# Kernel tuning notes

Measured on AMD Instinct MI355X. Metric: run time of the kernel, lower is better.

## Reference

```python
import jax, jax.numpy as jnp
import numpy as np

NUM_HEADS = 16
NEG = -10000000.0


def setup_inputs() -> dict:
    key = jax.random.key(0)
    k1, k2, k3 = jax.random.split(key, 3)
    B, N, C = 4, 2048, 1024
    inputs = jax.random.normal(k1, (B, N, C), dtype=jnp.float32)
    # learned params (xavier-ish scale)
    W_qkv = jax.random.normal(k2, (C, 3 * C), dtype=jnp.float32) * 0.02
    W_proj = jax.random.normal(k3, (C, C), dtype=jnp.float32) * 0.02
    b_proj = jnp.zeros((C,), dtype=jnp.float32)
    attn_mask = jnp.ones((N, N), dtype=jnp.int32)      # >0 means keep
    padding_mask = jnp.zeros((B, N), dtype=jnp.int32)  # >0 means mask out
    return {"inputs": inputs, "attn_mask": attn_mask, "padding_mask": padding_mask,
            "W_qkv": W_qkv, "W_proj": W_proj, "b_proj": b_proj}


def reference(inputs, attn_mask, padding_mask, W_qkv, W_proj, b_proj):
    B, N, C = inputs.shape
    H = NUM_HEADS
    d = C // H
    scale = d ** -0.5
    qkv = inputs @ W_qkv                                   # [B,N,3C]
    qkv = qkv.reshape(B, N, 3, H, d).transpose(2, 0, 3, 1, 4)  # [3,B,H,N,d]
    q, k, v = qkv[0], qkv[1], qkv[2]
    scores = jnp.einsum('bhqd,bhkd->bhqk', q, k) * scale   # [B,H,N,N]
    scores = jnp.where(attn_mask > 0, scores, NEG)
    pm = padding_mask[:, None, None, :]                    # [B,1,1,N]
    scores = jnp.where(pm > 0, NEG, scores)
    attn = jax.nn.softmax(scores, axis=-1)
    x = jnp.einsum('bhqk,bhkd->bhqd', attn, v)             # [B,H,N,d]
    x = x.swapaxes(1, 2).reshape(B, N, C)
    return x @ W_proj + b_proj
```

## Files before the change

### kernel.cpp

```cpp
#include <hip/hip_runtime.h>

#define NEG -10000000.0f
#define QSCALE 0.18033688011112042f

typedef __attribute__((ext_vector_type(8))) short bf16x8;
typedef __attribute__((ext_vector_type(4))) float f32x4;

static __device__ __forceinline__ short f2bf(float f) {
    unsigned int u = __float_as_uint(f);
    unsigned int r = (u + 0x7fffu + ((u >> 16) & 1u)) >> 16;
    return (short)r;
}

static __device__ __forceinline__ unsigned pack_bf16_2(float a, float b) {
    unsigned ua = __float_as_uint(a) + 0x8000u;
    unsigned ub = __float_as_uint(b) + 0x8000u;
    return __builtin_amdgcn_perm(ub, ua, 0x07060302u);
}

static __device__ __forceinline__ void async_cp16(const void* g, void* l) {
    __builtin_amdgcn_global_load_lds(
        (const __attribute__((address_space(1))) unsigned int*)g,
        (__attribute__((address_space(3))) unsigned int*)l, 16, 0, 0);
}

__global__ void cvt_bf16(const float* __restrict__ src, short* __restrict__ dst, int n4) {
    int i = blockIdx.x * blockDim.x + threadIdx.x;
    if (i < n4) {
        float4 v = reinterpret_cast<const float4*>(src)[i];
        short4 o;
        o.x = f2bf(v.x); o.y = f2bf(v.y); o.z = f2bf(v.z); o.w = f2bf(v.w);
        reinterpret_cast<short4*>(dst)[i] = o;
    }
}

__global__ void transpose_cvt(const float* __restrict__ src, short* __restrict__ dst,
                              int rows, int cols) {
    __shared__ float tile[32][33];
    int bx = blockIdx.x * 32;
    int by = blockIdx.y * 32;
    int tx = threadIdx.x & 31, ty = threadIdx.x >> 5;
    for (int j = 0; j < 4; ++j)
        tile[ty + j * 8][tx] = src[(size_t)(by + ty + j * 8) * cols + bx + tx];
    __syncthreads();
    for (int j = 0; j < 4; ++j)
        dst[(size_t)(bx + ty + j * 8) * rows + by + tx] = f2bf(tile[tx][ty + j * 8]);
}

__global__ void mask_flags(const int* __restrict__ attn_mask,
                           const int* __restrict__ padding, int* __restrict__ flags) {
    int blk = blockIdx.x;
    int tid = threadIdx.x;
    if (blk == 512) {
        if (tid < 128) {
            int b = tid >> 5, kt = tid & 31;
            int any = 0;
            for (int j = 0; j < 64; ++j) any |= (padding[b * 2048 + kt * 64 + j] > 0);
            flags[512 + tid] = any;
        }
        return;
    }
    int qt = blk >> 5, kt = blk & 31;
    __shared__ int blockok;
    if (tid == 0) blockok = 1;
    __syncthreads();
    int ok = 1;
    for (int j = 0; j < 32; ++j) {
        int idx = j * 256 + tid;
        int qr = qt * 128 + (idx >> 6);
        int kc = kt * 64 + (idx & 63);
        ok &= (attn_mask[(size_t)qr * 2048 + kc] != 0);
    }
    if (!ok) blockok = 0;
    __syncthreads();
    if (tid == 0) flags[blk] = blockok;
}

__global__ __launch_bounds__(256, 2) void gemm_bf16(
    const short* __restrict__ A, const short* __restrict__ Bt, int mode,
    short* __restrict__ q_ws, short* __restrict__ k_ws, short* __restrict__ v_ws,
    float* __restrict__ out, const float* __restrict__ bias) {
    const int K = 1024;
    __shared__ __align__(16) short smem[2][128][64];
    short (*As)[64] = smem[0];
    short (*Bs)[64] = smem[1];
    int tid = threadIdx.x, lane = tid & 63, w = tid >> 6;
    int wm = w & 1, wn = w >> 1;

    int nwg = gridDim.x * gridDim.y;
    int hw = blockIdx.y * gridDim.x + blockIdx.x;
    int logical = (hw & 7) * (nwg >> 3) + (hw >> 3);
    int bx = logical % gridDim.x, by = logical / gridDim.x;
    int m0 = by * 128, n0 = bx * 128;

    int col = lane & 15, quad = lane >> 4;
    int l8 = lane >> 3, j8 = lane & 7;

    f32x4 acc[4][4] = {};

    for (int k0 = 0; k0 < K; k0 += 64) {
        for (int c = 0; c < 4; ++c) {
            int rr = w * 32 + c * 8 + l8;
            int sw = (j8 ^ (rr & 7)) << 3;
            async_cp16(&A[(size_t)(m0 + rr) * K + k0 + sw], &As[w * 32 + c * 8][0]);
            async_cp16(&Bt[(size_t)(n0 + rr) * K + k0 + sw], &Bs[w * 32 + c * 8][0]);
        }
        __syncthreads();
        for (int ks = 0; ks < 2; ++ks) {
            bf16x8 af[4], bfr[4];
            for (int mt = 0; mt < 4; ++mt)
                af[mt] = *reinterpret_cast<const bf16x8*>(
                    &As[wm * 64 + mt * 16 + col][((ks * 4 + quad) ^ (col & 7)) << 3]);
            for (int nt = 0; nt < 4; ++nt)
                bfr[nt] = *reinterpret_cast<const bf16x8*>(
                    &Bs[wn * 64 + nt * 16 + col][((ks * 4 + quad) ^ (col & 7)) << 3]);
            for (int mt = 0; mt < 4; ++mt)
                for (int nt = 0; nt < 4; ++nt)
                    acc[mt][nt] = __builtin_amdgcn_mfma_f32_16x16x32_bf16(af[mt], bfr[nt], acc[mt][nt], 0, 0, 0);
        }
        __syncthreads();
    }

    short* L = &smem[0][0][0];

    if (mode == 0) {
        int which = n0 >> 10;
        int cb = n0 & 1023;
        int b = m0 >> 11, nb = m0 & 2047, hb = cb >> 6;
        if (which == 2) {
            for (int mt = 0; mt < 4; ++mt)
                for (int nt = 0; nt < 4; ++nt) {
                    int ml = wm * 64 + mt * 16 + quad * 4;
                    int cl = wn * 64 + nt * 16 + col;
                    int mp = (ml + 8 * cl) & 127;
                    short4 pk;
                    for (int r = 0; r < 4; ++r) ((short*)&pk)[r] = f2bf(acc[mt][nt][r]);
                    *reinterpret_cast<short4*>(&L[cl * 128 + mp]) = pk;
                }
            __syncthreads();
            for (int it = 0; it < 8; ++it) {
                int chunk = it * 256 + tid;
                int c = chunk >> 4, j = chunk & 15;
                int h = hb + (c >> 6), dd = c & 63;
                int4 val = *reinterpret_cast<const int4*>(&L[c * 128 + (((j + c) & 15) << 3)]);
                *reinterpret_cast<int4*>(
                    &v_ws[((size_t)((b * 16 + h) * 64 + dd)) * 2048 + nb + j * 8]) = val;
            }
        } else {
            short* dst = (which == 0) ? q_ws : k_ws;
            float scl = (which == 0) ? QSCALE : 1.0f;
            for (int mt = 0; mt < 4; ++mt)
                for (int nt = 0; nt < 4; ++nt)
                    for (int r = 0; r < 4; ++r) {
                        int ml = wm * 64 + mt * 16 + quad * 4 + r;
                        int cl = wn * 64 + nt * 16 + col;
                        L[ml * 128 + ((cl + 8 * ml) & 127)] = f2bf(acc[mt][nt][r] * scl);
                    }
            __syncthreads();
            for (int it = 0; it < 8; ++it) {
                int chunk = it * 256 + tid;
                int row = chunk >> 4, j = chunk & 15;
                int h = hb + (j >> 3), dd = (j & 7) * 8;
                int4 val = *reinterpret_cast<const int4*>(&L[row * 128 + (((j + row) & 15) << 3)]);
                *reinterpret_cast<int4*>(
                    &dst[((size_t)(b * 16 + h) * 2048 + nb + row) * 64 + dd]) = val;
            }
        }
    } else {
        float* Lf = reinterpret_cast<float*>(L);
        for (int half = 0; half < 2; ++half) {
            if (wm == half) {
                for (int mt = 0; mt < 4; ++mt)
                    for (int nt = 0; nt < 4; ++nt)
                        for (int r = 0; r < 4; ++r) {
                            int ml = mt * 16 + quad * 4 + r;
                            int cl = wn * 64 + nt * 16 + col;
                            Lf[ml * 128 + cl] = acc[mt][nt][r];
                        }
            }
            __syncthreads();
            for (int it = 0; it < 8; ++it) {
                int chunk = it * 256 + tid;
                int row = chunk >> 5, j = chunk & 31;
                float4 val = *reinterpret_cast<const float4*>(&Lf[row * 128 + j * 4]);
                float4 bv = *reinterpret_cast<const float4*>(&bias[n0 + j * 4]);
                val.x += bv.x; val.y += bv.y; val.z += bv.z; val.w += bv.w;
                *reinterpret_cast<float4*>(
                    &out[(size_t)(m0 + half * 64 + row) * 1024 + n0 + j * 4]) = val;
            }
            __syncthreads();
        }
    }
}

__global__ __launch_bounds__(256, 4) void flash_attn(
    const short* __restrict__ q_ws, const short* __restrict__ k_ws,
    const short* __restrict__ v_ws, const int* __restrict__ aflags,
    const int* __restrict__ pflags, const int* __restrict__ padding,
    const int* __restrict__ attn_mask, short* __restrict__ xb) {
    const int Nn = 2048, D = 64;
    __shared__ __align__(16) short QP[128][64];
    __shared__ __align__(16) short Ks[2][64][64];
    __shared__ __align__(16) short Vt[64][64];

    int tid = threadIdx.x, lane = tid & 63, w = tid >> 6;
    int col = lane & 15, quad = lane >> 4;

    int hw = blockIdx.y * 16 + blockIdx.x;
    int logical = (hw & 7) * 128 + (hw >> 3);
    int bh = logical >> 4, qt = logical & 15;
    int b = bh >> 4, h = bh & 15;
    int q0 = qt * 128;

    int l8 = lane >> 3, j8 = lane & 7;

    unsigned amask = (unsigned)__ballot(aflags[qt * 32 + (lane & 31)] != 0);
    unsigned pmask = (unsigned)__ballot(pflags[b * 32 + (lane & 31)] != 0);

    for (int c = 0; c < 4; ++c) {
        int rr = w * 32 + c * 8 + l8;
        async_cp16(&q_ws[((size_t)bh * Nn + q0 + rr) * D + ((j8 ^ (rr & 7)) << 3)],
                   &QP[w * 32 + c * 8][0]);
    }
    {
        int rr0 = w * 16 + l8, rr1 = w * 16 + 8 + l8;
        int s0 = (j8 ^ (rr0 & 7)) << 3, s1 = (j8 ^ (rr1 & 7)) << 3;
        async_cp16(&k_ws[((size_t)bh * Nn + rr0) * D + s0], &Ks[0][w * 16][0]);
        async_cp16(&k_ws[((size_t)bh * Nn + rr1) * D + s1], &Ks[0][w * 16 + 8][0]);
        async_cp16(&v_ws[((size_t)bh * D + rr0) * Nn + s0], &Vt[w * 16][0]);
        async_cp16(&v_ws[((size_t)bh * D + rr1) * Nn + s1], &Vt[w * 16 + 8][0]);
    }
    __syncthreads();

    bf16x8 qf[2][2];
    for (int t = 0; t < 2; ++t)
        for (int ks = 0; ks < 2; ++ks)
            qf[t][ks] = *reinterpret_cast<const bf16x8*>(
                &QP[w * 32 + t * 16 + col][((ks * 4 + quad) ^ (col & 7)) << 3]);

    f32x4 oacc[2][4] = {};
    f32x4 lacc[2] = {};

    for (int kt = 0; kt < 32; ++kt) {
        int k0 = kt * 64;
        int ktn = (kt < 31) ? kt + 1 : 31;

        if (kt) {
            asm volatile("s_waitcnt vmcnt(2)" ::: "memory");
            __builtin_amdgcn_s_barrier();
            __builtin_amdgcn_sched_barrier(0);
        }
        const short (*Kc)[64] = Ks[kt & 1];

        f32x4 sacc[4][2] = {};
        for (int ks = 0; ks < 2; ++ks) {
            bf16x8 kf[4];
            for (int mt = 0; mt < 4; ++mt)
                kf[mt] = *reinterpret_cast<const bf16x8*>(
                    &Kc[mt * 16 + col][((ks * 4 + quad) ^ (col & 7)) << 3]);
            __builtin_amdgcn_s_setprio(1);
            for (int mt = 0; mt < 4; ++mt)
                for (int t = 0; t < 2; ++t)
                    sacc[mt][t] = __builtin_amdgcn_mfma_f32_16x16x32_bf16(kf[mt], qf[t][ks], sacc[mt][t], 0, 0, 0);
            __builtin_amdgcn_s_setprio(0);
        }

        {
            int rr0 = w * 16 + l8, rr1 = w * 16 + 8 + l8;
            size_t kb = (size_t)bh * Nn + ktn * 64;
            async_cp16(&k_ws[(kb + rr0) * D + ((j8 ^ (rr0 & 7)) << 3)], &Ks[(kt + 1) & 1][w * 16][0]);
            async_cp16(&k_ws[(kb + rr1) * D + ((j8 ^ (rr1 & 7)) << 3)], &Ks[(kt + 1) & 1][w * 16 + 8][0]);
        }

        if (!((amask >> kt) & 1)) {
            for (int mt = 0; mt < 4; ++mt)
                for (int t = 0; t < 2; ++t)
                    for (int r = 0; r < 4; ++r) {
                        int kc = k0 + mt * 16 + quad * 4 + r;
                        int qr = q0 + w * 32 + t * 16 + col;
                        if (attn_mask[(size_t)qr * Nn + kc] == 0) sacc[mt][t][r] = NEG;
                    }
        }
        if ((pmask >> kt) & 1) {
            for (int mt = 0; mt < 4; ++mt)
                for (int r = 0; r < 4; ++r) {
                    int kc = k0 + mt * 16 + quad * 4 + r;
                    float pb = (padding[b * Nn + kc] > 0) ? NEG : 0.f;
                    for (int t = 0; t < 2; ++t) sacc[mt][t][r] += pb;
                }
        }

        for (int t = 0; t < 2; ++t) {
            int qrow = w * 32 + t * 16 + col;
            for (int mt = 0; mt < 4; ++mt) {
                f32x4 e;
                e[0] = __builtin_amdgcn_exp2f(sacc[mt][t][0]);
                e[1] = __builtin_amdgcn_exp2f(sacc[mt][t][1]);
                e[2] = __builtin_amdgcn_exp2f(sacc[mt][t][2]);
                e[3] = __builtin_amdgcn_exp2f(sacc[mt][t][3]);
                lacc[t] += e;
                unsigned p0 = pack_bf16_2(e[0], e[1]);
                unsigned p1 = pack_bf16_2(e[2], e[3]);
                int chunk = (mt * 2 + (quad >> 1)) ^ (col & 7);
                *reinterpret_cast<uint2*>(&QP[qrow][(chunk << 3) + ((quad & 1) << 2)]) =
                    make_uint2(p0, p1);
            }
        }

        if (kt) {
            asm volatile("s_waitcnt vmcnt(2)" ::: "memory");
            __builtin_amdgcn_s_barrier();
            __builtin_amdgcn_sched_barrier(0);
        }

        for (int ks = 0; ks < 2; ++ks) {
            bf16x8 pf[2], vf[4];
            for (int t = 0; t < 2; ++t)
                pf[t] = *reinterpret_cast<const bf16x8*>(
                    &QP[w * 32 + t * 16 + col][((ks * 4 + quad) ^ (col & 7)) << 3]);
            for (int nt = 0; nt < 4; ++nt)
                vf[nt] = *reinterpret_cast<const bf16x8*>(
                    &Vt[nt * 16 + col][((ks * 4 + quad) ^ (col & 7)) << 3]);
            __builtin_amdgcn_s_setprio(1);
            for (int t = 0; t < 2; ++t)
                for (int nt = 0; nt < 4; ++nt)
                    oacc[t][nt] = __builtin_amdgcn_mfma_f32_16x16x32_bf16(pf[t], vf[nt], oacc[t][nt], 0, 0, 0);
            __builtin_amdgcn_s_setprio(0);
        }

        asm volatile("s_waitcnt lgkmcnt(0)" ::: "memory");
        __builtin_amdgcn_sched_barrier(0);
        __builtin_amdgcn_s_barrier();
        {
            int rr0 = w * 16 + l8, rr1 = w * 16 + 8 + l8;
            size_t vb0 = ((size_t)bh * D + rr0) * Nn + ktn * 64;
            size_t vb1 = ((size_t)bh * D + rr1) * Nn + ktn * 64;
            async_cp16(&v_ws[vb0 + ((j8 ^ (rr0 & 7)) << 3)], &Vt[w * 16][0]);
            async_cp16(&v_ws[vb1 + ((j8 ^ (rr1 & 7)) << 3)], &Vt[w * 16 + 8][0]);
        }
    }

    for (int t = 0; t < 2; ++t) {
        float ls = lacc[t][0] + lacc[t][1] + lacc[t][2] + lacc[t][3];
        ls += __shfl_xor(ls, 16);
        ls += __shfl_xor(ls, 32);
        for (int r = 0; r < 4; ++r) {
            float lv = __shfl(ls, quad * 4 + r, 16);
            float inv = 1.f / lv;
            int n = q0 + w * 32 + t * 16 + quad * 4 + r;
            for (int nt = 0; nt < 4; ++nt) {
                int dd = nt * 16 + col;
                xb[((size_t)(b * Nn + n)) * 1024 + h * 64 + dd] = f2bf(oacc[t][nt][r] * inv);
            }
        }
    }
}

extern "C" void kernel_launch(void* const* d_in, const int* in_sizes, int n_in,
                              void* d_out, int out_size, void* d_ws, size_t ws_size,
                              hipStream_t stream) {
    const float* x        = (const float*)d_in[0];
    const int* attn_mask  = (const int*)d_in[1];
    const int* padding    = (const int*)d_in[2];
    const float* W_qkv    = (const float*)d_in[3];
    const float* W_proj   = (const float*)d_in[4];
    const float* b_proj   = (const float*)d_in[5];
    float* out            = (float*)d_out;

    char* ws = (char*)d_ws;
    short* Xb   = (short*)(ws);
    short* Wqt  = (short*)(ws + (16u << 20));
    short* Wpt  = (short*)(ws + (22u << 20));
    short* q_ws = (short*)(ws + (24u << 20));
    short* k_ws = (short*)(ws + (40u << 20));
    short* v_ws = (short*)(ws + (56u << 20));
    short* xbuf = (short*)(ws + (72u << 20));
    int*  flags = (int*)(ws + (88u << 20));

    cvt_bf16<<<8192, 256, 0, stream>>>(x, Xb, 8388608 / 4);
    transpose_cvt<<<dim3(3072 / 32, 1024 / 32), 256, 0, stream>>>(W_qkv, Wqt, 1024, 3072);
    transpose_cvt<<<dim3(1024 / 32, 1024 / 32), 256, 0, stream>>>(W_proj, Wpt, 1024, 1024);
    mask_flags<<<513, 256, 0, stream>>>(attn_mask, padding, flags);

    gemm_bf16<<<dim3(3072 / 128, 8192 / 128), 256, 0, stream>>>(
        Xb, Wqt, 0, q_ws, k_ws, v_ws, nullptr, nullptr);

    flash_attn<<<dim3(16, 64), 256, 0, stream>>>(
        q_ws, k_ws, v_ws, flags, flags + 512, padding, attn_mask, xbuf);

    gemm_bf16<<<dim3(1024 / 128, 8192 / 128), 256, 0, stream>>>(
        xbuf, Wpt, 1, nullptr, nullptr, nullptr, out, b_proj);
}
```

Measured before the change: 328.1 us.

## Restructure K/V async-load schedule in flash attention loop with plain barriers

Replaces the hand-tuned waitcnt/s_barrier pipeline with a simpler schedule. Each iteration now issues the current V tile load and the next K tile prefetch at the top of the loop, and uses __syncthreads before the PV stage and at the end of the iteration. The intent is to get more overlap for both loads behind the QK^T MFMAs and softmax, and to drop the separate trailing V prefetch barrier. The cost is that __syncthreads waits on all outstanding vector-memory ops, so V latency is no longer hidden across a full iteration. The explicit 16-byte alignment on the LDS buffers is also removed.

After: 328.2 us. About the same (+0.0%).

```diff
diff --git a/kernel.cpp b/kernel.cpp
--- a/kernel.cpp
+++ b/kernel.cpp
@@ -199,9 +199,9 @@
     const int* __restrict__ pflags, const int* __restrict__ padding,
     const int* __restrict__ attn_mask, short* __restrict__ xb) {
     const int Nn = 2048, D = 64;
-    __shared__ __align__(16) short QP[128][64];
-    __shared__ __align__(16) short Ks[2][64][64];
-    __shared__ __align__(16) short Vt[64][64];
+    __shared__ short QP[128][64];
+    __shared__ short Ks[2][64][64];
+    __shared__ short Vt[64][64];
 
     int tid = threadIdx.x, lane = tid & 63, w = tid >> 6;
     int col = lane & 15, quad = lane >> 4;
@@ -222,13 +222,10 @@
         async_cp16(&q_ws[((size_t)bh * Nn + q0 + rr) * D + ((j8 ^ (rr & 7)) << 3)],
                    &QP[w * 32 + c * 8][0]);
     }
-    {
-        int rr0 = w * 16 + l8, rr1 = w * 16 + 8 + l8;
-        int s0 = (j8 ^ (rr0 & 7)) << 3, s1 = (j8 ^ (rr1 & 7)) << 3;
-        async_cp16(&k_ws[((size_t)bh * Nn + rr0) * D + s0], &Ks[0][w * 16][0]);
-        async_cp16(&k_ws[((size_t)bh * Nn + rr1) * D + s1], &Ks[0][w * 16 + 8][0]);
-        async_cp16(&v_ws[((size_t)bh * D + rr0) * Nn + s0], &Vt[w * 16][0]);
-        async_cp16(&v_ws[((size_t)bh * D + rr1) * Nn + s1], &Vt[w * 16 + 8][0]);
+    for (int c = 0; c < 2; ++c) {
+        int rr = w * 16 + c * 8 + l8;
+        int sw = (j8 ^ (rr & 7)) << 3;
+        async_cp16(&k_ws[((size_t)bh * Nn + rr) * D + sw], &Ks[0][w * 16 + c * 8][0]);
     }
     __syncthreads();
 
@@ -243,33 +240,33 @@
 
     for (int kt = 0; kt < 32; ++kt) {
         int k0 = kt * 64;
-        int ktn = (kt < 31) ? kt + 1 : 31;
-
-        if (kt) {
-            asm volatile("s_waitcnt vmcnt(2)" ::: "memory");
-            __builtin_amdgcn_s_barrier();
-            __builtin_amdgcn_sched_barrier(0);
-        }
-        const short (*Kc)[64] = Ks[kt & 1];
+        int cur = kt & 1;
+
+        for (int c = 0; c < 2; ++c) {
+            int rr = w * 16 + c * 8 + l8;
+            int sw = (j8 ^ (rr & 7)) << 3;
+            async_cp16(&v_ws[((size_t)bh * D + rr) * Nn + k0 + sw], &Vt[w * 16 + c * 8][0]);
+        }
+        if (kt < 31) {
+            for (int c = 0; c < 2; ++c) {
+                int rr = w * 16 + c * 8 + l8;
+                int sw = (j8 ^ (rr & 7)) << 3;
+                async_cp16(&k_ws[((size_t)bh * Nn + k0 + 64 + rr) * D + sw],
+                           &Ks[cur ^ 1][w * 16 + c * 8][0]);
+            }
+        }
 
         f32x4 sacc[4][2] = {};
         for (int ks = 0; ks < 2; ++ks) {
             bf16x8 kf[4];
             for (int mt = 0; mt < 4; ++mt)
                 kf[mt] = *reinterpret_cast<const bf16x8*>(
-                    &Kc[mt * 16 + col][((ks * 4 + quad) ^ (col & 7)) << 3]);
+                    &Ks[cur][mt * 16 + col][((ks * 4 + quad) ^ (col & 7)) << 3]);
             __builtin_amdgcn_s_setprio(1);
             for (int mt = 0; mt < 4; ++mt)
                 for (int t = 0; t < 2; ++t)
                     sacc[mt][t] = __builtin_amdgcn_mfma_f32_16x16x32_bf16(kf[mt], qf[t][ks], sacc[mt][t], 0, 0, 0);
             __builtin_amdgcn_s_setprio(0);
-        }
-
-        {
-            int rr0 = w * 16 + l8, rr1 = w * 16 + 8 + l8;
-            size_t kb = (size_t)bh * Nn + ktn * 64;
-            async_cp16(&k_ws[(kb + rr0) * D + ((j8 ^ (rr0 & 7)) << 3)], &Ks[(kt + 1) & 1][w * 16][0]);
-            async_cp16(&k_ws[(kb + rr1) * D + ((j8 ^ (rr1 & 7)) << 3)], &Ks[(kt + 1) & 1][w * 16 + 8][0]);
         }
 
         if (!((amask >> kt) & 1)) {
@@ -307,11 +304,7 @@
             }
         }
 
-        if (kt) {
-            asm volatile("s_waitcnt vmcnt(2)" ::: "memory");
-            __builtin_amdgcn_s_barrier();
-            __builtin_amdgcn_sched_barrier(0);
-        }
+        __syncthreads();
 
         for (int ks = 0; ks < 2; ++ks) {
             bf16x8 pf[2], vf[4];
@@ -327,17 +320,7 @@
                     oacc[t][nt] = __builtin_amdgcn_mfma_f32_16x16x32_bf16(pf[t], vf[nt], oacc[t][nt], 0, 0, 0);
             __builtin_amdgcn_s_setprio(0);
         }
-
-        asm volatile("s_waitcnt lgkmcnt(0)" ::: "memory");
-        __builtin_amdgcn_sched_barrier(0);
-        __builtin_amdgcn_s_barrier();
-        {
-            int rr0 = w * 16 + l8, rr1 = w * 16 + 8 + l8;
-            size_t vb0 = ((size_t)bh * D + rr0) * Nn + ktn * 64;
-            size_t vb1 = ((size_t)bh * D + rr1) * Nn + ktn * 64;
-            async_cp16(&v_ws[vb0 + ((j8 ^ (rr0 & 7)) << 3)], &Vt[w * 16][0]);
-            async_cp16(&v_ws[vb1 + ((j8 ^ (rr1 & 7)) << 3)], &Vt[w * 16 + 8][0]);
-        }
+        __syncthreads();
     }
 
     for (int t = 0; t < 2; ++t) {
```
